# Optimization experiments

Hardware: AMD Instinct MI355X
Metric: run time of the kernel (lower is better)

The kernel has to match this reference:

```python
import jax, jax.numpy as jnp
import numpy as np
from functools import partial

B, D, E, O, K = 65536, 64, 16, 512, 2  # batch, feat dim, num_experts, output_size, top-k


def setup_inputs() -> dict:
    key = jax.random.key(0)
    k1, k2, k3, k4, k5 = jax.random.split(key, 5)
    scale_g = 1.0 / np.sqrt(D)
    return {
        "x": jax.random.normal(k1, (B, D), dtype=jnp.float32),
        "wg": jax.random.uniform(k2, (D, E), dtype=jnp.float32, minval=-scale_g, maxval=scale_g),
        "bg": jnp.zeros((E,), dtype=jnp.float32),
        "We": jax.random.uniform(k3, (E, D, O), dtype=jnp.float32, minval=-scale_g, maxval=scale_g),
        "be": jax.random.uniform(k4, (E, O), dtype=jnp.float32, minval=-scale_g, maxval=scale_g),
    }


def reference(x, wg, bg, We, be):
    # --- gating (noisy_gating=False / eval path) ---
    logits = jax.nn.softmax(x @ wg + bg, axis=1)            # [B, E]
    top_vals, top_idx = jax.lax.top_k(logits, K)            # [B, K]
    top_gates = top_vals / (jnp.sum(top_vals, axis=1, keepdims=True) + 1e-6)
    rows = jnp.arange(x.shape[0])[:, None]                  # [B, 1]
    gates = jnp.zeros_like(logits).at[rows, top_idx].set(top_gates)  # dense [B, E], sparse rows

    # --- dispatch / per-expert linear / gated scatter-combine ---
    # Equivalent dense-masked form of SparseDispatcher: y[i] = sum_e gates[i,e] * (x[i] @ We[e] + be[e])
    def step(y, ewb):
        w, b, g = ewb                                       # [D,O], [O], [B]
        return y + g[:, None] * (x @ w + b), None

    y0 = jnp.zeros((x.shape[0], We.shape[2]), dtype=x.dtype)
    y, _ = jax.lax.scan(step, y0, (We, be, gates.T))
    return y
```

## Files before the change

kernel.cpp:

```cpp
#include <hip/hip_runtime.h>

typedef unsigned int u32;
typedef unsigned short u16;
typedef float f4 __attribute__((ext_vector_type(4)));
typedef __bf16 b8 __attribute__((ext_vector_type(8)));
typedef unsigned short us8 __attribute__((ext_vector_type(8)));

#define DD 64
#define NE 16
#define OO 512
#define TR 64

struct __align__(16) Tile { u32 pid, slot, nr, pad; };

union U8 { us8 u; b8 b; };

__device__ __forceinline__ u16 f2bf(float f) {
  u32 u = __float_as_uint(f);
  u32 r = (u + 0x7fffu + ((u >> 16) & 1u)) >> 16;
  return (u16)r;
}

__global__ void k_front(const float* __restrict__ We, u16* __restrict__ WeT,
                        const float* __restrict__ x, const float* __restrict__ wg,
                        const float* __restrict__ bg, u32* __restrict__ hist_t,
                        u32* __restrict__ pid_arr, float* __restrict__ glo_arr,
                        float* __restrict__ ghi_arr) {
  __shared__ float tl[64][65];
  __shared__ u32 hcnt[256];
  int t = threadIdx.x;

  if (blockIdx.x < 128) {
    int b = blockIdx.x;
    int e = b >> 3;
    int oc = (b & 7) * 64;
    int d = t >> 2, seg = (t & 3) * 16;
    const f4* src = (const f4*)(We + ((size_t)(e * DD + d)) * OO + oc + seg);
    f4 v0 = src[0], v1 = src[1], v2 = src[2], v3 = src[3];
#pragma unroll
    for (int j = 0; j < 4; j++) {
      tl[d][seg + j]      = v0[j];
      tl[d][seg + 4 + j]  = v1[j];
      tl[d][seg + 8 + j]  = v2[j];
      tl[d][seg + 12 + j] = v3[j];
    }
    __syncthreads();
    int o = t >> 2, ds = (t & 3) * 16;
    us8 o0, o1;
#pragma unroll
    for (int j = 0; j < 8; j++) {
      o0[j] = f2bf(tl[ds + j][o]);
      o1[j] = f2bf(tl[ds + 8 + j][o]);
    }
    u16* dst = WeT + ((size_t)(e * OO + oc + o)) * DD + ds;
    *(us8*)dst = o0;
    *(us8*)(dst + 8) = o1;
    return;
  }

  int gb = blockIdx.x - 128;
  hcnt[t] = 0;
  __syncthreads();
  int row = gb * 256 + t;

  float l[NE];
#pragma unroll
  for (int e = 0; e < NE; e++) l[e] = bg[e];

  const f4* xp = (const f4*)(x + (size_t)row * DD);
  for (int d4 = 0; d4 < 16; d4++) {
    f4 xv = xp[d4];
#pragma unroll
    for (int qq = 0; qq < 4; qq++) {
      float xs = xv[qq];
      const float* wrow = wg + (d4 * 4 + qq) * NE;
#pragma unroll
      for (int e = 0; e < NE; e++) l[e] = fmaf(xs, wrow[e], l[e]);
    }
  }
  float mx = l[0];
#pragma unroll
  for (int e = 1; e < NE; e++) mx = fmaxf(mx, l[e]);
  float Z = 0.f;
#pragma unroll
  for (int e = 0; e < NE; e++) Z += __expf(l[e] - mx);
  int i1 = 0; float b1 = l[0];
#pragma unroll
  for (int e = 1; e < NE; e++) { if (l[e] > b1) { b1 = l[e]; i1 = e; } }
  int i2 = -1; float b2 = -1e30f;
#pragma unroll
  for (int e = 0; e < NE; e++) { if (e != i1 && l[e] > b2) { b2 = l[e]; i2 = e; } }
  float p1 = __expf(b1 - mx) / Z;
  float p2 = __expf(b2 - mx) / Z;
  float den = p1 + p2 + 1e-6f;
  float g1 = p1 / den, g2 = p2 / den;
  int elo, ehi; float glo, ghi;
  if (i1 < i2) { elo = i1; ehi = i2; glo = g1; ghi = g2; }
  else         { elo = i2; ehi = i1; glo = g2; ghi = g1; }
  u32 pid = (u32)(elo * NE + ehi);
  pid_arr[row] = pid;
  glo_arr[row] = glo;
  ghi_arr[row] = ghi;
  atomicAdd(&hcnt[pid], 1u);
  __syncthreads();
  hist_t[t * 256 + gb] = hcnt[t];
}

__global__ void k_colscan_t(u32* __restrict__ hist_t, u32* __restrict__ tot) {
  __shared__ u32 s[256];
  int b = threadIdx.x, p = blockIdx.x;
  u32 v = hist_t[p * 256 + b];
  s[b] = v;
  __syncthreads();
  for (int d = 1; d < 256; d <<= 1) {
    u32 a = 0;
    if (b >= d) a = s[b - d];
    __syncthreads();
    s[b] += a;
    __syncthreads();
  }
  hist_t[p * 256 + b] = s[b] - v;
  if (b == 255) tot[p] = s[255];
}

__global__ void k_base(const u32* __restrict__ tot, u32* __restrict__ base,
                       u32* __restrict__ ntp, Tile* __restrict__ tiles) {
  __shared__ u32 s[256], s2[256];
  int t = threadIdx.x;
  u32 v = tot[t];
  u32 nt = (v + (TR - 1)) >> 6;
  s[t] = v; s2[t] = nt;
  __syncthreads();
  for (int d = 1; d < 256; d <<= 1) {
    u32 a = 0, c = 0;
    if (t >= d) { a = s[t - d]; c = s2[t - d]; }
    __syncthreads();
    s[t] += a; s2[t] += c;
    __syncthreads();
  }
  u32 rb = s[t] - v;
  u32 tb = s2[t] - nt;
  base[t] = rb;
  for (u32 k = 0; k < nt; k++) {
    Tile td;
    td.pid = (u32)t;
    td.slot = rb + k * (u32)TR;
    u32 rem = v - k * (u32)TR;
    td.nr = rem < (u32)TR ? rem : (u32)TR;
    td.pad = 0;
    tiles[tb + k] = td;
  }
  if (t == 255) *ntp = s2[255];
}

__global__ void k_scatter(const u32* __restrict__ pid_arr, const u32* __restrict__ hist_t,
                          const u32* __restrict__ base, u32* __restrict__ sorted) {
  __shared__ u32 lcnt[256], lbase[256];
  int t = threadIdx.x;
  lcnt[t] = 0;
  lbase[t] = base[t];
  __syncthreads();
  int row = blockIdx.x * 256 + t;
  u32 pid = pid_arr[row];
  u32 rank = atomicAdd(&lcnt[pid], 1u);
  u32 off = lbase[pid] + hist_t[pid * 256 + blockIdx.x];
  sorted[off + rank] = (u32)row;
}

__global__ __launch_bounds__(256, 3)
void k_moe(const float* __restrict__ x, const u16* __restrict__ WeT,
           const float* __restrict__ be, const u32* __restrict__ sorted,
           const u32* __restrict__ ntp, const Tile* __restrict__ tiles,
           const float* __restrict__ glo_arr, const float* __restrict__ ghi_arr,
           float* __restrict__ y) {
  __shared__ __align__(16) u16 Xl[TR * 72];
  __shared__ u32 rid_s[TR];
  __shared__ float glo_s[TR], ghi_s[TR];

  u32 bid = blockIdx.x;
  if (bid >= *ntp) return;
  Tile td = tiles[bid];
  u32 e_lo = td.pid >> 4, e_hi = td.pid & 15u;
  u32 slot0 = td.slot, nr = td.nr;

  int t = threadIdx.x;
  if (t < TR) {
    u32 i = (u32)t;
    u32 slot = slot0 + ((i < nr) ? i : 0u);
    u32 r = sorted[slot];
    rid_s[t] = r;
    bool valid = i < nr;
    glo_s[t] = valid ? glo_arr[r] : 0.f;
    ghi_s[t] = valid ? ghi_arr[r] : 0.f;
  }
  __syncthreads();
  {
    int i = t >> 2;
    int seg = (t & 3) * 16;
    u32 r = rid_s[i];
    const f4* xp = (const f4*)(x + (size_t)r * DD + seg);
    f4 v0 = xp[0], v1 = xp[1], v2 = xp[2], v3 = xp[3];
    float vv[16] = { v0[0], v0[1], v0[2], v0[3], v1[0], v1[1], v1[2], v1[3],
                     v2[0], v2[1], v2[2], v2[3], v3[0], v3[1], v3[2], v3[3] };
    us8 o0, o1;
#pragma unroll
    for (int j = 0; j < 8; j++) { o0[j] = f2bf(vv[j]); o1[j] = f2bf(vv[8 + j]); }
    *(us8*)&Xl[i * 72 + seg] = o0;
    *(us8*)&Xl[i * 72 + seg + 8] = o1;
  }
  __syncthreads();

  int lane = t & 63;
  int w = t >> 6;
  int q = lane >> 4;
  int ln = lane & 15;

  b8 xfr[4][2];
#pragma unroll
  for (int rt = 0; rt < 4; rt++)
#pragma unroll
    for (int kc = 0; kc < 2; kc++) {
      U8 tmp; tmp.u = *(const us8*)&Xl[(rt * 16 + ln) * 72 + kc * 32 + q * 8];
      xfr[rt][kc] = tmp.b;
    }

  float gl[4], gh[4];
  bool vld[4];
  float* yp[4];
#pragma unroll
  for (int rt = 0; rt < 4; rt++) {
    int i = rt * 16 + ln;
    gl[rt] = glo_s[i];
    gh[rt] = ghi_s[i];
    vld[rt] = (u32)i < nr;
    yp[rt] = y + (size_t)rid_s[i] * OO;
  }

  const u16* wlo = WeT + (size_t)e_lo * OO * DD;
  const u16* whi = WeT + (size_t)e_hi * OO * DD;
  const f4 zero = {0.f, 0.f, 0.f, 0.f};

#pragma unroll 2
  for (int ct = 0; ct < 8; ct++) {
    int colA = w * 128 + ct * 16 + ln;
    int colq = w * 128 + ct * 16 + q * 4;
    const us8* plo = (const us8*)(wlo + (size_t)colA * DD + q * 8);
    const us8* phi = (const us8*)(whi + (size_t)colA * DD + q * 8);
    U8 t0, t1, t2, t3;
    t0.u = plo[0]; t1.u = plo[4];
    t2.u = phi[0]; t3.u = phi[4];
    b8 wl0 = t0.b, wl1 = t1.b, wh0 = t2.b, wh1 = t3.b;
    f4 bl = *(const f4*)(be + e_lo * OO + colq);
    f4 bh = *(const f4*)(be + e_hi * OO + colq);

#pragma unroll
    for (int rt = 0; rt < 4; rt++) {
      f4 aL = zero, aH = zero;
      aL = __builtin_amdgcn_mfma_f32_16x16x32_bf16(wl0, xfr[rt][0], aL, 0, 0, 0);
      aL = __builtin_amdgcn_mfma_f32_16x16x32_bf16(wl1, xfr[rt][1], aL, 0, 0, 0);
      aH = __builtin_amdgcn_mfma_f32_16x16x32_bf16(wh0, xfr[rt][0], aH, 0, 0, 0);
      aH = __builtin_amdgcn_mfma_f32_16x16x32_bf16(wh1, xfr[rt][1], aH, 0, 0, 0);
      if (vld[rt]) {
        f4 v;
#pragma unroll
        for (int r = 0; r < 4; r++)
          v[r] = gl[rt] * (aL[r] + bl[r]) + gh[rt] * (aH[r] + bh[r]);
        *(f4*)(yp[rt] + colq) = v;
      }
    }
  }
}

extern "C" void kernel_launch(void* const* d_in, const int* in_sizes, int n_in,
                              void* d_out, int out_size, void* d_ws, size_t ws_size,
                              hipStream_t stream) {
  const float* x  = (const float*)d_in[0];
  const float* wg = (const float*)d_in[1];
  const float* bg = (const float*)d_in[2];
  const float* We = (const float*)d_in[3];
  const float* be = (const float*)d_in[4];
  float* y = (float*)d_out;

  char* ws = (char*)d_ws;
  u32* ntp     = (u32*)(ws + 0);
  Tile* tiles  = (Tile*)(ws + 4096);
  u32* pid_arr = (u32*)(ws + 32768);
  float* glo_a = (float*)(ws + 32768 + 262144);
  float* ghi_a = (float*)(ws + 32768 + 2 * 262144);
  u32* sorted  = (u32*)(ws + 32768 + 3 * 262144);
  u16* WeT     = (u16*)(ws + 32768 + 4 * 262144);
  u32* hist_t  = (u32*)(ws + 32768 + 4 * 262144 + 1048576);
  u32* tot     = (u32*)(ws + 32768 + 4 * 262144 + 1048576 + 262144);
  u32* base    = (u32*)(ws + 32768 + 4 * 262144 + 1048576 + 262144 + 1024);

  k_front<<<384, 256, 0, stream>>>(We, WeT, x, wg, bg, hist_t, pid_arr, glo_a, ghi_a);
  k_colscan_t<<<256, 256, 0, stream>>>(hist_t, tot);
  k_base<<<1, 256, 0, stream>>>(tot, base, ntp, tiles);
  k_scatter<<<256, 256, 0, stream>>>(pid_arr, hist_t, base, sorted);
  k_moe<<<1144, 256, 0, stream>>>(x, WeT, be, sorted, ntp, tiles, glo_a, ghi_a, y);
}
```

Before: 197.8 us.

## Fuse colscan, base and scatter kernels into one grid-synchronized meta kernel

Merges three small metadata kernels (per-pair column scan, global base/tile construction, and row scatter) into a single 256-block kernel. The blocks meet at a software grid barrier built on an atomic counter that k_front resets, and then every block recomputes the global prefix redundantly. The aim is to cut two kernel launches and their gaps. The barrier relies on all 256 blocks being resident at once, which should hold on this GPU, and each block now repeats the global scan.

Result: slower. 206.9 us (+4.6%).

```diff
diff --git a/kernel.cpp b/kernel.cpp
--- a/kernel.cpp
+++ b/kernel.cpp
@@ -25,12 +25,13 @@
                         const float* __restrict__ x, const float* __restrict__ wg,
                         const float* __restrict__ bg, u32* __restrict__ hist_t,
                         u32* __restrict__ pid_arr, float* __restrict__ glo_arr,
-                        float* __restrict__ ghi_arr) {
+                        float* __restrict__ ghi_arr, u32* __restrict__ cnt) {
   __shared__ float tl[64][65];
   __shared__ u32 hcnt[256];
   int t = threadIdx.x;
 
   if (blockIdx.x < 128) {
+    if (blockIdx.x == 0 && t == 0) *cnt = 0u;
     int b = blockIdx.x;
     int e = b >> 3;
     int oc = (b & 7) * 64;
@@ -106,30 +107,40 @@
   hist_t[t * 256 + gb] = hcnt[t];
 }
 
-__global__ void k_colscan_t(u32* __restrict__ hist_t, u32* __restrict__ tot) {
-  __shared__ u32 s[256];
-  int b = threadIdx.x, p = blockIdx.x;
-  u32 v = hist_t[p * 256 + b];
-  s[b] = v;
+__global__ __launch_bounds__(256)
+void k_meta(u32* __restrict__ hist_t, u32* __restrict__ tot, u32* __restrict__ cnt,
+            u32* __restrict__ ntp, Tile* __restrict__ tiles,
+            const u32* __restrict__ pid_arr, u32* __restrict__ sorted) {
+  __shared__ u32 s[256], s2[256], sbase[256], lcnt[256];
+  __shared__ u32 lastf;
+  int t = threadIdx.x, p = blockIdx.x;
+
+  u32 v = hist_t[p * 256 + t];
+  s[t] = v;
   __syncthreads();
   for (int d = 1; d < 256; d <<= 1) {
     u32 a = 0;
-    if (b >= d) a = s[b - d];
-    __syncthreads();
-    s[b] += a;
-    __syncthreads();
-  }
-  hist_t[p * 256 + b] = s[b] - v;
-  if (b == 255) tot[p] = s[255];
-}
-
-__global__ void k_base(const u32* __restrict__ tot, u32* __restrict__ base,
-                       u32* __restrict__ ntp, Tile* __restrict__ tiles) {
-  __shared__ u32 s[256], s2[256];
-  int t = threadIdx.x;
-  u32 v = tot[t];
-  u32 nt = (v + (TR - 1)) >> 6;
-  s[t] = v; s2[t] = nt;
+    if (t >= d) a = s[t - d];
+    __syncthreads();
+    s[t] += a;
+    __syncthreads();
+  }
+  hist_t[p * 256 + t] = s[t] - v;
+  if (t == 255) tot[p] = s[255];
+  __syncthreads();
+
+  if (t == 0) {
+    __threadfence();
+    u32 old = atomicAdd(cnt, 1u);
+    lastf = (old == 255u) ? 1u : 0u;
+    while (atomicAdd(cnt, 0u) < 256u) __builtin_amdgcn_s_sleep(2);
+    __threadfence();
+  }
+  __syncthreads();
+
+  u32 tv = tot[t];
+  u32 nt = (tv + (TR - 1)) >> 6;
+  s[t] = tv; s2[t] = nt;
   __syncthreads();
   for (int d = 1; d < 256; d <<= 1) {
     u32 a = 0, c = 0;
@@ -138,32 +149,28 @@
     s[t] += a; s2[t] += c;
     __syncthreads();
   }
-  u32 rb = s[t] - v;
-  u32 tb = s2[t] - nt;
-  base[t] = rb;
-  for (u32 k = 0; k < nt; k++) {
-    Tile td;
-    td.pid = (u32)t;
-    td.slot = rb + k * (u32)TR;
-    u32 rem = v - k * (u32)TR;
-    td.nr = rem < (u32)TR ? rem : (u32)TR;
-    td.pad = 0;
-    tiles[tb + k] = td;
-  }
-  if (t == 255) *ntp = s2[255];
-}
-
-__global__ void k_scatter(const u32* __restrict__ pid_arr, const u32* __restrict__ hist_t,
-                          const u32* __restrict__ base, u32* __restrict__ sorted) {
-  __shared__ u32 lcnt[256], lbase[256];
-  int t = threadIdx.x;
+  sbase[t] = s[t] - tv;
+  if (lastf) {
+    u32 rb = s[t] - tv, tb = s2[t] - nt;
+    for (u32 kk = 0; kk < nt; kk++) {
+      Tile td;
+      td.pid = (u32)t;
+      td.slot = rb + kk * (u32)TR;
+      u32 rem = tv - kk * (u32)TR;
+      td.nr = rem < (u32)TR ? rem : (u32)TR;
+      td.pad = 0;
+      tiles[tb + kk] = td;
+    }
+    if (t == 255) *ntp = s2[255];
+  }
+  __syncthreads();
+
   lcnt[t] = 0;
-  lbase[t] = base[t];
-  __syncthreads();
-  int row = blockIdx.x * 256 + t;
+  __syncthreads();
+  int row = p * 256 + t;
   u32 pid = pid_arr[row];
   u32 rank = atomicAdd(&lcnt[pid], 1u);
-  u32 off = lbase[pid] + hist_t[pid * 256 + blockIdx.x];
+  u32 off = sbase[pid] + hist_t[pid * 256 + p];
   sorted[off + rank] = (u32)row;
 }
 
@@ -283,6 +290,7 @@
 
   char* ws = (char*)d_ws;
   u32* ntp     = (u32*)(ws + 0);
+  u32* cnt     = (u32*)(ws + 64);
   Tile* tiles  = (Tile*)(ws + 4096);
   u32* pid_arr = (u32*)(ws + 32768);
   float* glo_a = (float*)(ws + 32768 + 262144);
@@ -291,11 +299,8 @@
   u16* WeT     = (u16*)(ws + 32768 + 4 * 262144);
   u32* hist_t  = (u32*)(ws + 32768 + 4 * 262144 + 1048576);
   u32* tot     = (u32*)(ws + 32768 + 4 * 262144 + 1048576 + 262144);
-  u32* base    = (u32*)(ws + 32768 + 4 * 262144 + 1048576 + 262144 + 1024);
-
-  k_front<<<384, 256, 0, stream>>>(We, WeT, x, wg, bg, hist_t, pid_arr, glo_a, ghi_a);
-  k_colscan_t<<<256, 256, 0, stream>>>(hist_t, tot);
-  k_base<<<1, 256, 0, stream>>>(tot, base, ntp, tiles);
-  k_scatter<<<256, 256, 0, stream>>>(pid_arr, hist_t, base, sorted);
+
+  k_front<<<384, 256, 0, stream>>>(We, WeT, x, wg, bg, hist_t, pid_arr, glo_a, ghi_a, cnt);
+  k_meta<<<256, 256, 0, stream>>>(hist_t, tot, cnt, ntp, tiles, pid_arr, sorted);
   k_moe<<<1144, 256, 0, stream>>>(x, WeT, be, sorted, ntp, tiles, glo_a, ghi_a, y);
 }
```
